# Kernel tuning notes

Hardware: AMD Instinct MI355X
Metric: run time of the kernel (lower is better)

The kernel has to match this reference:

```python
import jax, jax.numpy as jnp
import numpy as np
import math

L, B, S, D, H, DI, V = 4, 2, 1024, 768, 12, 3072, 512
DK = D // H

def gelu_tanh(x):
    c = math.sqrt(2.0 / math.pi)
    return 0.5 * x * (1.0 + jnp.tanh(c * (x + 0.044715 * x ** 3)))

def layer_norm(x, g, b, eps=1e-5):
    mu = jnp.mean(x, axis=-1, keepdims=True)
    var = jnp.var(x, axis=-1, keepdims=True)
    return (x - mu) * jax.lax.rsqrt(var + eps) * g + b

def setup_inputs() -> dict:
    key = jax.random.key(0)
    ks = jax.random.split(key, 12)
    w = 0.02  # init scale
    return {
        "x": jax.random.randint(ks[0], (B, S), 0, V),
        "embed": jax.random.normal(ks[1], (V, D), jnp.float32) * w,
        "pos_emb": jax.random.normal(ks[2], (S, D), jnp.float32) * w,
        "ln1_g": jnp.ones((L, D), jnp.float32),
        "ln1_b": jnp.zeros((L, D), jnp.float32),
        "wq": jax.random.normal(ks[3], (L, D, D), jnp.float32) * w,
        "bq": jnp.zeros((L, D), jnp.float32),
        "wk": jax.random.normal(ks[4], (L, D, D), jnp.float32) * w,
        "bk": jnp.zeros((L, D), jnp.float32),
        "wv": jax.random.normal(ks[5], (L, D, D), jnp.float32) * w,
        "bv": jnp.zeros((L, D), jnp.float32),
        "wo": jax.random.normal(ks[6], (L, D, D), jnp.float32) * w,
        "bo": jnp.zeros((L, D), jnp.float32),
        "ln2_g": jnp.ones((L, D), jnp.float32),
        "ln2_b": jnp.zeros((L, D), jnp.float32),
        "w_in": jax.random.normal(ks[7], (L, D, DI), jnp.float32) * w,
        "b_in": jnp.zeros((L, DI), jnp.float32),
        "w_out": jax.random.normal(ks[8], (L, DI, D), jnp.float32) * w,
        "b_out": jnp.zeros((L, D), jnp.float32),
        "lnf_g": jnp.ones((D,), jnp.float32),
        "lnf_b": jnp.zeros((D,), jnp.float32),
        "out_w": jax.random.normal(ks[9], (D, V), jnp.float32) * w,
    }

def reference(x, embed, pos_emb, ln1_g, ln1_b, wq, bq, wk, bk, wv, bv, wo, bo,
              ln2_g, ln2_b, w_in, b_in, w_out, b_out, lnf_g, lnf_b, out_w):
    s = x.shape[1]
    h = embed[x] + pos_emb[None, :s]                       # [B,S,D]
    causal = jnp.tril(jnp.ones((s, s), bool))              # True = keep
    scale = 1.0 / math.sqrt(DK)
    for l in range(L):
        a = layer_norm(h, ln1_g[l], ln1_b[l])
        q = (a @ wq[l] + bq[l]).reshape(-1, s, H, DK)
        k = (a @ wk[l] + bk[l]).reshape(-1, s, H, DK)
        v = (a @ wv[l] + bv[l]).reshape(-1, s, H, DK)
        scores = jnp.einsum('bqhd,bkhd->bhqk', q, k) * scale
        scores = jnp.where(causal, scores, -jnp.inf)
        attn = jax.nn.softmax(scores, axis=-1)
        o = jnp.einsum('bhqk,bkhd->bqhd', attn, v).reshape(-1, s, D)
        h = h + o @ wo[l] + bo[l]
        f = layer_norm(h, ln2_g[l], ln2_b[l])
        h = h + gelu_tanh(f @ w_in[l] + b_in[l]) @ w_out[l] + b_out[l]
    h = layer_norm(h, lnf_g, lnf_b)
    return h @ out_w                                       # [B,S,V] logits
```

## Files before the change

kernel.cpp:

```cpp
#include <hip/hip_runtime.h>
#include <hip/hip_bf16.h>


#define TKN    2048
#define DMODEL 768
#define SEQ    1024
#define NH     12
#define DHEAD  64
#define DFF    3072
#define NL     4
#define NVOCAB 512
#define NQKV   2304

typedef unsigned short u16;
typedef __attribute__((ext_vector_type(4))) float f32x4;
typedef __attribute__((ext_vector_type(8))) short short8;
typedef __attribute__((ext_vector_type(4))) unsigned short us4;

__device__ __forceinline__ u16 f2bf(float f) {
  unsigned u = __builtin_bit_cast(unsigned, f);
  u += 0x7fffu + ((u >> 16) & 1u);
  return (u16)(u >> 16);
}

__device__ __forceinline__ float bf2f(u16 u) {
  unsigned v = ((unsigned)u) << 16;
  return __builtin_bit_cast(float, v);
}

__device__ __forceinline__ u16 bf_eighth(u16 u) {
  int e = (u >> 7) & 0xFF;
  return e >= 3 ? (u16)(u - (3 << 7)) : (u16)(u & 0x8000);
}

__device__ __forceinline__ short8 mk8(us4 lo, us4 hi) {
  short8 r;
  r[0] = (short)lo[0]; r[1] = (short)lo[1]; r[2] = (short)lo[2]; r[3] = (short)lo[3];
  r[4] = (short)hi[0]; r[5] = (short)hi[1]; r[6] = (short)hi[2]; r[7] = (short)hi[3];
  return r;
}

__device__ __forceinline__ void gload16(const u16* g, u16* l) {
  __builtin_amdgcn_global_load_lds(
      (const __attribute__((address_space(1))) unsigned int*)g,
      (__attribute__((address_space(3))) unsigned int*)l, 16, 0, 0);
}

__global__ __launch_bounds__(256) void k_embed(const int* __restrict__ x,
                                               const float* __restrict__ emb,
                                               const float* __restrict__ pos,
                                               float* __restrict__ h) {
  int t = blockIdx.x;
  int s = t & (SEQ - 1);
  int id = x[t];
  int d = threadIdx.x;
#pragma unroll
  for (int j = 0; j < 3; ++j, d += 256)
    h[t * DMODEL + d] = emb[id * DMODEL + d] + pos[s * DMODEL + d];
}

__global__ __launch_bounds__(256) void k_ln(const float* __restrict__ h,
                                            const float* __restrict__ gam,
                                            const float* __restrict__ bet,
                                            u16* __restrict__ out) {
  __shared__ float sbuf[8];
  int row = blockIdx.x, tid = threadIdx.x;
  const float* hr = h + (size_t)row * DMODEL;
  float x0 = hr[tid], x1 = hr[tid + 256], x2 = hr[tid + 512];
  float s = x0 + x1 + x2;
#pragma unroll
  for (int off = 32; off > 0; off >>= 1) s += __shfl_down(s, off);
  if ((tid & 63) == 0) sbuf[tid >> 6] = s;
  __syncthreads();
  float mu = (sbuf[0] + sbuf[1] + sbuf[2] + sbuf[3]) * (1.0f / DMODEL);
  float d0 = x0 - mu, d1 = x1 - mu, d2 = x2 - mu;
  float v = d0 * d0 + d1 * d1 + d2 * d2;
#pragma unroll
  for (int off = 32; off > 0; off >>= 1) v += __shfl_down(v, off);
  if ((tid & 63) == 0) sbuf[4 + (tid >> 6)] = v;
  __syncthreads();
  float var = (sbuf[4] + sbuf[5] + sbuf[6] + sbuf[7]) * (1.0f / DMODEL);
  float rstd = rsqrtf(var + 1e-5f);
  size_t o = (size_t)row * DMODEL;
  out[o + tid]       = f2bf(d0 * rstd * gam[tid]       + bet[tid]);
  out[o + tid + 256] = f2bf(d1 * rstd * gam[tid + 256] + bet[tid + 256]);
  out[o + tid + 512] = f2bf(d2 * rstd * gam[tid + 512] + bet[tid + 512]);
}

__device__ __forceinline__ void cvt_tile(const float* __restrict__ src, int ldS,
                                         int k0, int n0src,
                                         u16* __restrict__ dst, int ldD, int n0dst,
                                         int tid, u16 (*tl)[72]) {
  int kr = tid >> 2, nj = (tid & 3) << 4;
  const float* sp = src + (size_t)(k0 + kr) * ldS + n0src + nj;
  float4 a0 = ((const float4*)sp)[0];
  float4 a1 = ((const float4*)sp)[1];
  float4 a2 = ((const float4*)sp)[2];
  float4 a3 = ((const float4*)sp)[3];
  u16* tr = &tl[kr][nj];
  tr[0]=f2bf(a0.x); tr[1]=f2bf(a0.y); tr[2]=f2bf(a0.z); tr[3]=f2bf(a0.w);
  tr[4]=f2bf(a1.x); tr[5]=f2bf(a1.y); tr[6]=f2bf(a1.z); tr[7]=f2bf(a1.w);
  tr[8]=f2bf(a2.x); tr[9]=f2bf(a2.y); tr[10]=f2bf(a2.z); tr[11]=f2bf(a2.w);
  tr[12]=f2bf(a3.x); tr[13]=f2bf(a3.y); tr[14]=f2bf(a3.z); tr[15]=f2bf(a3.w);
  __syncthreads();
  int nr = tid >> 2, kj = (tid & 3) << 4;
  us4 o[4];
#pragma unroll
  for (int c = 0; c < 4; ++c)
#pragma unroll
    for (int i = 0; i < 4; ++i) o[c][i] = tl[kj + c * 4 + i][nr];
  u16* dp = dst + (size_t)(n0dst + nr) * ldD + k0 + kj;
  ((us4*)dp)[0] = o[0]; ((us4*)dp)[1] = o[1];
  ((us4*)dp)[2] = o[2]; ((us4*)dp)[3] = o[3];
}

__global__ __launch_bounds__(256) void k_cvtL(const float* __restrict__ wq,
                                              const float* __restrict__ wk,
                                              const float* __restrict__ wv,
                                              const float* __restrict__ wo,
                                              const float* __restrict__ win,
                                              const float* __restrict__ wout,
                                              u16* __restrict__ wqkvT,
                                              u16* __restrict__ woT,
                                              u16* __restrict__ winT,
                                              u16* __restrict__ woutT) {
  __shared__ u16 tl[64][72];
  int t = blockIdx.x, tid = threadIdx.x;
  if (t < 432) {
    int kt = t % 12, ntile = t / 12;
    int gn0 = ntile * 64, sel = gn0 / DMODEL;
    const float* src = sel == 0 ? wq : sel == 1 ? wk : wv;
    cvt_tile(src, DMODEL, kt * 64, gn0 - sel * DMODEL, wqkvT, DMODEL, gn0, tid, tl);
  } else if (t < 576) {
    int t2 = t - 432, kt = t2 % 12, nt = t2 / 12;
    cvt_tile(wo, DMODEL, kt * 64, nt * 64, woT, DMODEL, nt * 64, tid, tl);
  } else if (t < 1152) {
    int t3 = t - 576, kt = t3 % 12, nt = t3 / 12;
    cvt_tile(win, DFF, kt * 64, nt * 64, winT, DMODEL, nt * 64, tid, tl);
  } else {
    int t4 = t - 1152, kt = t4 % 48, nt = t4 / 48;
    cvt_tile(wout, DMODEL, kt * 64, nt * 64, woutT, DFF, nt * 64, tid, tl);
  }
}

__global__ __launch_bounds__(256) void k_cvtT(const float* __restrict__ src,
                                              u16* __restrict__ dst,
                                              int K, int N) {
  __shared__ u16 tl[64][72];
  cvt_tile(src, N, blockIdx.x * 64, blockIdx.y * 64, dst, K, blockIdx.y * 64,
           threadIdx.x, tl);
}

__global__ __launch_bounds__(256) void k_packb(const float* __restrict__ bq,
                                               const float* __restrict__ bk,
                                               const float* __restrict__ bv,
                                               float* __restrict__ dst) {
  int i = blockIdx.x * 256 + threadIdx.x;
  if (i < NL * NQKV) {
    int l = i / NQKV, j = i - l * NQKV;
    float v = j < DMODEL ? bq[l * DMODEL + j]
            : j < 2 * DMODEL ? bk[l * DMODEL + j - DMODEL]
            : bv[l * DMODEL + j - 2 * DMODEL];
    dst[i] = v;
  }
}

template <int EP, int BM, int BN>
__global__ __launch_bounds__(256) void k_mm(const u16* __restrict__ A,
                                            const u16* __restrict__ BT,
                                            const float* __restrict__ bias,
                                            void* __restrict__ outp,
                                            int N, int K) {
  constexpr int MI = BM / 32;
  constexpr int NJ = BN / 32;
  __shared__ __align__(16) u16 As[2][BM * 64];
  __shared__ __align__(16) u16 Bs[2][BN * 64];
  const int nbx = gridDim.x;
  int lin = blockIdx.y * nbx + blockIdx.x;
  const int chunk = (nbx * gridDim.y) >> 3;
  lin = (lin & 7) * chunk + (lin >> 3);
  const int bn = (lin % nbx) * BN, bm = (lin / nbx) * BM;

  const int tid = threadIdx.x, lane = tid & 63, wid = tid >> 6;
  const int g = lane >> 4, fl = lane & 15;
  const int wm = wid >> 1, wn = wid & 1;

  const int srow = wid * 8 + (lane >> 3);
  const int scol = ((lane & 7) ^ (lane >> 3)) << 3;
  const u16* ag = A + (size_t)(bm + srow) * K + scol;
  const u16* bg = BT + (size_t)(bn + srow) * K + scol;

  f32x4 acc[MI][NJ] = {};
  const int sw = (fl & 7) << 4;

  auto stage = [&](int buf, int kk) {
#pragma unroll
    for (int is = 0; is < MI; ++is)
      gload16(ag + kk + (size_t)is * 32 * K, &As[buf][wid * 512 + is * 2048]);
#pragma unroll
    for (int is = 0; is < NJ; ++is)
      gload16(bg + kk + (size_t)is * 32 * K, &Bs[buf][wid * 512 + is * 2048]);
  };

  const int ks = K / gridDim.z;
  const int kb0 = blockIdx.z * ks;
  const int nk = ks >> 6;
  stage(0, kb0);
  __syncthreads();
  int cur = 0;
  for (int kt = 0; kt < nk; ++kt) {
    if (kt + 1 < nk) stage(cur ^ 1, kb0 + ((kt + 1) << 6));
#pragma unroll
    for (int k0 = 0; k0 < 64; k0 += 32) {
      const int bo = (k0 + 4 * g) * 2;
      short8 af[MI], bf[NJ];
#pragma unroll
      for (int i = 0; i < MI; ++i) {
        const char* base = (const char*)&As[cur][(wm * (BM / 2) + i * 16 + fl) * 64];
        af[i] = mk8(*(const us4*)(base + (bo ^ sw)),
                    *(const us4*)(base + ((bo + 32) ^ sw)));
      }
#pragma unroll
      for (int j = 0; j < NJ; ++j) {
        const char* base = (const char*)&Bs[cur][(wn * (BN / 2) + j * 16 + fl) * 64];
        bf[j] = mk8(*(const us4*)(base + (bo ^ sw)),
                    *(const us4*)(base + ((bo + 32) ^ sw)));
      }
#pragma unroll
      for (int i = 0; i < MI; ++i)
#pragma unroll
        for (int j = 0; j < NJ; ++j)
          acc[i][j] = __builtin_amdgcn_mfma_f32_16x16x32_bf16(af[i], bf[j], acc[i][j], 0, 0, 0);
    }
    __syncthreads();
    cur ^= 1;
  }

  const int row0 = bm + wm * (BM / 2) + 4 * g;
  const int col0 = bn + wn * (BN / 2) + fl;
#pragma unroll
  for (int j = 0; j < NJ; ++j) {
    int col = col0 + j * 16;
    float bv = (EP == 3) ? 0.0f : bias[col];
    if (EP == 1 && blockIdx.z != 0) bv = 0.0f;
#pragma unroll
    for (int i = 0; i < MI; ++i) {
#pragma unroll
      for (int r = 0; r < 4; ++r) {
        int row = row0 + i * 16 + r;
        float val = acc[i][j][r] + bv;
        size_t idx = (size_t)row * N + col;
        if (EP == 0) {
          ((u16*)outp)[idx] = f2bf(val);
        } else if (EP == 1) {
          atomicAdd(&((float*)outp)[idx], val);
        } else if (EP == 2) {
          float t = 0.7978845608028654f * (val + 0.044715f * val * val * val);
          ((u16*)outp)[idx] = f2bf(0.5f * val * (1.0f + tanhf(t)));
        } else {
          ((float*)outp)[idx] = val;
        }
      }
    }
  }
}

__global__ __launch_bounds__(256) void k_attn(const u16* __restrict__ qkv,
                                              u16* __restrict__ pO,
                                              float* __restrict__ pML) {
  __shared__ u16 Vt[2][DHEAD * 68];
  int bid = blockIdx.x;
  int lin = (bid & 7) * 120 + (bid >> 3);
  const int bh = lin / 40;
  const int idx = lin - bh * 40;
  int qb, sp;
  if (idx < 4)       { qb = idx;                     sp = 0; }
  else if (idx < 12) { qb = 4 + ((idx - 4) >> 1);    sp = (idx - 4) & 1; }
  else if (idx < 24) { int t = idx - 12; qb = 8 + t / 3;  sp = t - (t / 3) * 3; }
  else               { int t = idx - 24; qb = 12 + (t >> 2); sp = t & 3; }
  const int nsp = 1 + (qb >> 2), nt = qb + 1;
  const int t_lo = sp * nt / nsp, t_hi = (sp + 1) * nt / nsp;

  const int b = bh / NH, hh = bh % NH;
  const int tid = threadIdx.x, lane = tid & 63, w = tid >> 6;
  const int g = lane >> 4, fl = lane & 15;
  const int qrow = qb * 64 + w * 16 + fl;
  const u16* qp = qkv + (size_t)(b * SEQ + qrow) * NQKV + hh * DHEAD;

  short8 qf[2];
#pragma unroll
  for (int hf = 0; hf < 2; ++hf) {
    us4 lo = *(const us4*)(qp + hf * 32 + 4 * g);
    us4 hi = *(const us4*)(qp + hf * 32 + 16 + 4 * g);
#pragma unroll
    for (int i = 0; i < 4; ++i) { lo[i] = bf_eighth(lo[i]); hi[i] = bf_eighth(hi[i]); }
    qf[hf] = mk8(lo, hi);
  }

  float m = -1e30f, lsum = 0.0f;
  f32x4 oacc[4] = {};
  const int vr = tid >> 2, vd = (tid & 3) << 4;
  const u16* vbase = qkv + (size_t)(b * SEQ + vr) * NQKV + 2 * DMODEL + hh * DHEAD + vd;
  const u16* kbase0 = qkv + (size_t)(b * SEQ) * NQKV + DMODEL + hh * DHEAD;

  {
    const u16* vp = vbase + (size_t)t_lo * 64 * NQKV;
    us4 vv[4];
#pragma unroll
    for (int qi = 0; qi < 4; ++qi) vv[qi] = *(const us4*)(vp + qi * 4);
#pragma unroll
    for (int qi = 0; qi < 4; ++qi)
#pragma unroll
      for (int i = 0; i < 4; ++i) Vt[0][(vd + qi * 4 + i) * 68 + vr] = vv[qi][i];
  }
  __syncthreads();
  int cur = 0;

  for (int t64 = t_lo; t64 < t_hi; ++t64) {
    const u16* kb64 = kbase0 + (size_t)t64 * 64 * NQKV;
    us4 kv[4][4];
#pragma unroll
    for (int q4 = 0; q4 < 4; ++q4) {
      const u16* kp = kb64 + (size_t)(q4 * 16 + fl) * NQKV;
#pragma unroll
      for (int j = 0; j < 4; ++j) kv[q4][j] = *(const us4*)(kp + j * 16 + 4 * g);
    }
    const bool pf = (t64 + 1 < t_hi);
    us4 vvn[4];
    if (pf) {
      const u16* vp = vbase + (size_t)(t64 + 1) * 64 * NQKV;
#pragma unroll
      for (int qi = 0; qi < 4; ++qi) vvn[qi] = *(const us4*)(vp + qi * 4);
    }

    f32x4 sfr[4];
    __builtin_amdgcn_s_setprio(1);
#pragma unroll
    for (int sub = 0; sub < 4; ++sub) {
      short8 kf0 = mk8(kv[sub][0], kv[sub][1]);
      short8 kf1 = mk8(kv[sub][2], kv[sub][3]);
      f32x4 s = {};
      s = __builtin_amdgcn_mfma_f32_16x16x32_bf16(kf0, qf[0], s, 0, 0, 0);
      s = __builtin_amdgcn_mfma_f32_16x16x32_bf16(kf1, qf[1], s, 0, 0, 0);
      sfr[sub] = s;
    }
    __builtin_amdgcn_s_setprio(0);

    float sc[16];
    if (t64 == qb) {
#pragma unroll
      for (int sub = 0; sub < 4; ++sub)
#pragma unroll
        for (int r = 0; r < 4; ++r) {
          int key = t64 * 64 + sub * 16 + 4 * g + r;
          sc[sub * 4 + r] = (key <= qrow) ? sfr[sub][r] : -1e30f;
        }
    } else {
#pragma unroll
      for (int sub = 0; sub < 4; ++sub)
#pragma unroll
        for (int r = 0; r < 4; ++r) sc[sub * 4 + r] = sfr[sub][r];
    }
    float pmax = sc[0];
#pragma unroll
    for (int e = 1; e < 16; ++e) pmax = fmaxf(pmax, sc[e]);
    pmax = fmaxf(pmax, __shfl_xor(pmax, 16));
    pmax = fmaxf(pmax, __shfl_xor(pmax, 32));

    float p[16];
    if (__all(pmax <= m + 8.0f)) {
      float ps = 0.0f;
#pragma unroll
      for (int e = 0; e < 16; ++e) { p[e] = __expf(sc[e] - m); ps += p[e]; }
      ps += __shfl_xor(ps, 16);
      ps += __shfl_xor(ps, 32);
      lsum += ps;
    } else {
      float mnew = fmaxf(m, pmax);
      float corr = __expf(m - mnew);
      float ps = 0.0f;
#pragma unroll
      for (int e = 0; e < 16; ++e) { p[e] = __expf(sc[e] - mnew); ps += p[e]; }
      ps += __shfl_xor(ps, 16);
      ps += __shfl_xor(ps, 32);
      lsum = lsum * corr + ps;
      m = mnew;
      float cr[4];
#pragma unroll
      for (int r = 0; r < 4; ++r) cr[r] = __shfl(corr, 4 * g + r);
#pragma unroll
      for (int nb = 0; nb < 4; ++nb)
#pragma unroll
        for (int r = 0; r < 4; ++r) oacc[nb][r] *= cr[r];
    }

    short8 pf0, pf1;
#pragma unroll
    for (int e = 0; e < 8; ++e) { pf0[e] = (short)f2bf(p[e]); pf1[e] = (short)f2bf(p[8 + e]); }

    __builtin_amdgcn_s_setprio(1);
#pragma unroll
    for (int nb = 0; nb < 4; ++nb) {
      const u16* vtp = &Vt[cur][(nb * 16 + fl) * 68 + 4 * g];
      short8 vf0 = mk8(*(const us4*)vtp, *(const us4*)(vtp + 16));
      short8 vf1 = mk8(*(const us4*)(vtp + 32), *(const us4*)(vtp + 48));
      oacc[nb] = __builtin_amdgcn_mfma_f32_16x16x32_bf16(pf0, vf0, oacc[nb], 0, 0, 0);
      oacc[nb] = __builtin_amdgcn_mfma_f32_16x16x32_bf16(pf1, vf1, oacc[nb], 0, 0, 0);
    }
    __builtin_amdgcn_s_setprio(0);

    if (pf) {
      __syncthreads();
#pragma unroll
      for (int qi = 0; qi < 4; ++qi)
#pragma unroll
        for (int i = 0; i < 4; ++i) Vt[cur ^ 1][(vd + qi * 4 + i) * 68 + vr] = vvn[qi][i];
      __syncthreads();
      cur ^= 1;
    }
  }

  const size_t part = ((size_t)bh * 16 + qb) * 4 + sp;
  u16* ob = pO + part * 4096;
  float* ml = pML + part * 128;
#pragma unroll
  for (int nb = 0; nb < 4; ++nb)
#pragma unroll
    for (int r = 0; r < 4; ++r)
      ob[(w * 16 + 4 * g + r) * 64 + nb * 16 + fl] = f2bf(oacc[nb][r]);
  if (g == 0) {
    ml[w * 16 + fl] = m;
    ml[64 + w * 16 + fl] = lsum;
  }
}

__global__ __launch_bounds__(256) void k_ared(const u16* __restrict__ pO,
                                              const float* __restrict__ pML,
                                              u16* __restrict__ O) {
  __shared__ float wgt[4][64];
  __shared__ float iLs[64];
  const int qb = blockIdx.x, bh = blockIdx.y;
  const int nsp = 1 + (qb >> 2);
  const int b = bh / NH, hh = bh % NH;
  const int tid = threadIdx.x;
  const size_t p0 = ((size_t)bh * 16 + qb) * 4;
  if (tid < 64) {
    float M = -1e30f;
    for (int s = 0; s < nsp; ++s) M = fmaxf(M, pML[(p0 + s) * 128 + tid]);
    float L = 0.0f;
    for (int s = 0; s < nsp; ++s) {
      float wv = __expf(pML[(p0 + s) * 128 + tid] - M);
      wgt[s][tid] = wv;
      L += pML[(p0 + s) * 128 + 64 + tid] * wv;
    }
    iLs[tid] = 1.0f / L;
  }
  __syncthreads();
  for (int i = tid; i < 4096; i += 256) {
    int row = i >> 6, d = i & 63;
    float acc = 0.0f;
    for (int s = 0; s < nsp; ++s)
      acc += bf2f(pO[(p0 + s) * 4096 + i]) * wgt[s][row];
    O[(size_t)(b * SEQ + qb * 64 + row) * DMODEL + hh * DHEAD + d] = f2bf(acc * iLs[row]);
  }
}

extern "C" void kernel_launch(void* const* d_in, const int* in_sizes, int n_in,
                              void* d_out, int out_size, void* d_ws, size_t ws_size,
                              hipStream_t stream) {
  const int*   x    = (const int*)d_in[0];
  const float* emb  = (const float*)d_in[1];
  const float* pos  = (const float*)d_in[2];
  const float* ln1g = (const float*)d_in[3];
  const float* ln1b = (const float*)d_in[4];
  const float* wq   = (const float*)d_in[5];
  const float* bq   = (const float*)d_in[6];
  const float* wk   = (const float*)d_in[7];
  const float* bk   = (const float*)d_in[8];
  const float* wv   = (const float*)d_in[9];
  const float* bv   = (const float*)d_in[10];
  const float* wo   = (const float*)d_in[11];
  const float* bo   = (const float*)d_in[12];
  const float* ln2g = (const float*)d_in[13];
  const float* ln2b = (const float*)d_in[14];
  const float* win  = (const float*)d_in[15];
  const float* bin  = (const float*)d_in[16];
  const float* wout = (const float*)d_in[17];
  const float* bout = (const float*)d_in[18];
  const float* lnfg = (const float*)d_in[19];
  const float* lnfb = (const float*)d_in[20];
  const float* outw = (const float*)d_in[21];

  char* w8 = (char*)d_ws;
  float* h    = (float*)(w8);
  u16* abuf   = (u16*)(w8 + 6291456);
  u16* qkv    = (u16*)(w8 + 9437184);
  u16* obuf   = (u16*)(w8 + 18874368);
  u16* ffbuf  = (u16*)(w8 + 9437184);
  u16* wqkvT  = (u16*)(w8 + 22020096);
  u16* woT    = (u16*)(w8 + 25559040);
  u16* winT   = (u16*)(w8 + 26738688);
  u16* woutT  = (u16*)(w8 + 31457280);
  u16* outwT  = (u16*)(w8 + 36175872);
  float* bqkv = (float*)(w8 + 36962304);
  u16* pO     = (u16*)(w8 + 36999168);
  float* pML  = (float*)(w8 + 6291456 + 0);

  pML = (float*)(w8 + 6291456);

  k_embed<<<TKN, 256, 0, stream>>>(x, emb, pos, h);
  k_packb<<<36, 256, 0, stream>>>(bq, bk, bv, bqkv);
  k_cvtT<<<dim3(12, 8), 256, 0, stream>>>(outw, outwT, DMODEL, NVOCAB);

  for (int l = 0; l < NL; ++l) {
    k_cvtL<<<1728, 256, 0, stream>>>(
        wq + (size_t)l * DMODEL * DMODEL, wk + (size_t)l * DMODEL * DMODEL,
        wv + (size_t)l * DMODEL * DMODEL, wo + (size_t)l * DMODEL * DMODEL,
        win + (size_t)l * DMODEL * DFF, wout + (size_t)l * DFF * DMODEL,
        wqkvT, woT, winT, woutT);

    k_ln<<<TKN, 256, 0, stream>>>(h, ln1g + l * DMODEL, ln1b + l * DMODEL, abuf);
    k_mm<0, 128, 64><<<dim3(NQKV / 64, TKN / 128, 1), 256, 0, stream>>>(
        abuf, wqkvT, bqkv + l * NQKV, qkv, NQKV, DMODEL);
    k_attn<<<960, 256, 0, stream>>>(qkv, pO, pML);
    k_ared<<<dim3(SEQ / 64, 2 * NH), 256, 0, stream>>>(pO, pML, obuf);
    k_mm<1, 128, 64><<<dim3(DMODEL / 64, TKN / 128, 2), 256, 0, stream>>>(
        obuf, woT, bo + l * DMODEL, h, DMODEL, DMODEL);
    k_ln<<<TKN, 256, 0, stream>>>(h, ln2g + l * DMODEL, ln2b + l * DMODEL, abuf);
    k_mm<2, 128, 64><<<dim3(DFF / 64, TKN / 128, 1), 256, 0, stream>>>(
        abuf, winT, bin + l * DFF, ffbuf, DFF, DMODEL);
    k_mm<1, 128, 64><<<dim3(DMODEL / 64, TKN / 128, 4), 256, 0, stream>>>(
        ffbuf, woutT, bout + l * DMODEL, h, DMODEL, DFF);
  }

  k_ln<<<TKN, 256, 0, stream>>>(h, lnfg, lnfb, abuf);
  k_mm<3, 64, 64><<<dim3(NVOCAB / 64, TKN / 64, 1), 256, 0, stream>>>(
      abuf, outwT, nullptr, d_out, NVOCAB, DMODEL);
}
```

Measured before the change: 713.3 us.

## Head-major QKV layout, finer attention split, batched weight conversion, single V buffer

The QKV GEMM epilogue now writes Q, K and V into separate head-major [b,h,s,64] buffers and folds the 1/8 softmax scale into Q, so attention no longer rescales Q per element and reads contiguous rows. Attention splits the KV range more finely (up to 8 partials per query block, 1728 blocks) to balance causal work, and the V tile drops from double-buffered to a single LDS buffer. Weight conversion for all layers is hoisted into one launch before the loop, which removes three launches but needs a larger workspace. The single V buffer may add stalls, and the extra partials add reduction traffic.

```diff
diff --git a/kernel.cpp b/kernel.cpp
--- a/kernel.cpp
+++ b/kernel.cpp
@@ -26,11 +26,6 @@
 __device__ __forceinline__ float bf2f(u16 u) {
   unsigned v = ((unsigned)u) << 16;
   return __builtin_bit_cast(float, v);
-}
-
-__device__ __forceinline__ u16 bf_eighth(u16 u) {
-  int e = (u >> 7) & 0xFF;
-  return e >= 3 ? (u16)(u - (3 << 7)) : (u16)(u & 0x8000);
 }
 
 __device__ __forceinline__ short8 mk8(us4 lo, us4 hi) {
@@ -125,21 +120,27 @@
                                               u16* __restrict__ winT,
                                               u16* __restrict__ woutT) {
   __shared__ u16 tl[64][72];
+  const int l = blockIdx.y;
+  const size_t wDD = (size_t)DMODEL * DMODEL, wDF = (size_t)DMODEL * DFF;
   int t = blockIdx.x, tid = threadIdx.x;
   if (t < 432) {
     int kt = t % 12, ntile = t / 12;
     int gn0 = ntile * 64, sel = gn0 / DMODEL;
-    const float* src = sel == 0 ? wq : sel == 1 ? wk : wv;
-    cvt_tile(src, DMODEL, kt * 64, gn0 - sel * DMODEL, wqkvT, DMODEL, gn0, tid, tl);
+    const float* src = (sel == 0 ? wq : sel == 1 ? wk : wv) + l * wDD;
+    cvt_tile(src, DMODEL, kt * 64, gn0 - sel * DMODEL,
+             wqkvT + l * (size_t)NQKV * DMODEL, DMODEL, gn0, tid, tl);
   } else if (t < 576) {
     int t2 = t - 432, kt = t2 % 12, nt = t2 / 12;
-    cvt_tile(wo, DMODEL, kt * 64, nt * 64, woT, DMODEL, nt * 64, tid, tl);
+    cvt_tile(wo + l * wDD, DMODEL, kt * 64, nt * 64,
+             woT + l * wDD, DMODEL, nt * 64, tid, tl);
   } else if (t < 1152) {
     int t3 = t - 576, kt = t3 % 12, nt = t3 / 12;
-    cvt_tile(win, DFF, kt * 64, nt * 64, winT, DMODEL, nt * 64, tid, tl);
+    cvt_tile(win + l * wDF, DFF, kt * 64, nt * 64,
+             winT + l * wDF, DMODEL, nt * 64, tid, tl);
   } else {
     int t4 = t - 1152, kt = t4 % 48, nt = t4 / 48;
-    cvt_tile(wout, DMODEL, kt * 64, nt * 64, woutT, DFF, nt * 64, tid, tl);
+    cvt_tile(wout + l * wDF, DMODEL, kt * 64, nt * 64,
+             woutT + l * wDF, DFF, nt * 64, tid, tl);
   }
 }
 
@@ -257,78 +258,91 @@
         } else if (EP == 2) {
           float t = 0.7978845608028654f * (val + 0.044715f * val * val * val);
           ((u16*)outp)[idx] = f2bf(0.5f * val * (1.0f + tanhf(t)));
+        } else if (EP == 3) {
+          ((float*)outp)[idx] = val;
         } else {
-          ((float*)outp)[idx] = val;
+          int sel = col / DMODEL;
+          int c = col - sel * DMODEL;
+          int hh2 = c >> 6, dk = c & 63;
+          int bb = row >> 10, ss = row & (SEQ - 1);
+          if (sel == 0) val *= 0.125f;
+          ((u16*)outp)[(size_t)sel * (TKN * DMODEL) +
+                       (((size_t)(bb * NH + hh2) * SEQ + ss) << 6) + dk] = f2bf(val);
         }
       }
     }
   }
 }
 
-__global__ __launch_bounds__(256) void k_attn(const u16* __restrict__ qkv,
+__global__ __launch_bounds__(256) void k_attn(const u16* __restrict__ qh,
                                               u16* __restrict__ pO,
                                               float* __restrict__ pML) {
-  __shared__ u16 Vt[2][DHEAD * 68];
+  __shared__ u16 Vt[DHEAD * 68];
   int bid = blockIdx.x;
-  int lin = (bid & 7) * 120 + (bid >> 3);
-  const int bh = lin / 40;
-  const int idx = lin - bh * 40;
-  int qb, sp;
-  if (idx < 4)       { qb = idx;                     sp = 0; }
-  else if (idx < 12) { qb = 4 + ((idx - 4) >> 1);    sp = (idx - 4) & 1; }
-  else if (idx < 24) { int t = idx - 12; qb = 8 + t / 3;  sp = t - (t / 3) * 3; }
-  else               { int t = idx - 24; qb = 12 + (t >> 2); sp = t & 3; }
-  const int nsp = 1 + (qb >> 2), nt = qb + 1;
+  int lin = (bid & 7) * 216 + (bid >> 3);
+  const int bh = lin / 72;
+  const int idx = lin - bh * 72;
+  int qb = 0, sp = 0, c = 0;
+#pragma unroll
+  for (int q = 0; q < 16; ++q) {
+    int n = 1 + (q >> 1);
+    if (idx >= c && idx < c + n) { qb = q; sp = idx - c; }
+    c += n;
+  }
+  const int nsp = 1 + (qb >> 1), nt = qb + 1;
   const int t_lo = sp * nt / nsp, t_hi = (sp + 1) * nt / nsp;
 
   const int b = bh / NH, hh = bh % NH;
+  const u16* kh = qh + TKN * DMODEL;
+  const u16* vh = qh + 2 * (TKN * DMODEL);
+  const size_t headbase = ((size_t)bh * SEQ) << 6;
+
   const int tid = threadIdx.x, lane = tid & 63, w = tid >> 6;
   const int g = lane >> 4, fl = lane & 15;
   const int qrow = qb * 64 + w * 16 + fl;
-  const u16* qp = qkv + (size_t)(b * SEQ + qrow) * NQKV + hh * DHEAD;
 
   short8 qf[2];
-#pragma unroll
-  for (int hf = 0; hf < 2; ++hf) {
-    us4 lo = *(const us4*)(qp + hf * 32 + 4 * g);
-    us4 hi = *(const us4*)(qp + hf * 32 + 16 + 4 * g);
-#pragma unroll
-    for (int i = 0; i < 4; ++i) { lo[i] = bf_eighth(lo[i]); hi[i] = bf_eighth(hi[i]); }
-    qf[hf] = mk8(lo, hi);
+  {
+    const u16* qp = qh + headbase + ((size_t)qrow << 6);
+#pragma unroll
+    for (int hf = 0; hf < 2; ++hf) {
+      us4 lo = *(const us4*)(qp + hf * 32 + 4 * g);
+      us4 hi = *(const us4*)(qp + hf * 32 + 16 + 4 * g);
+      qf[hf] = mk8(lo, hi);
+    }
   }
 
   float m = -1e30f, lsum = 0.0f;
   f32x4 oacc[4] = {};
   const int vr = tid >> 2, vd = (tid & 3) << 4;
-  const u16* vbase = qkv + (size_t)(b * SEQ + vr) * NQKV + 2 * DMODEL + hh * DHEAD + vd;
-  const u16* kbase0 = qkv + (size_t)(b * SEQ) * NQKV + DMODEL + hh * DHEAD;
+  const u16* vbase = vh + headbase + ((size_t)vr << 6) + vd;
+  const u16* kbase = kh + headbase;
 
   {
-    const u16* vp = vbase + (size_t)t_lo * 64 * NQKV;
+    const u16* vp = vbase + ((size_t)t_lo << 12);
     us4 vv[4];
 #pragma unroll
     for (int qi = 0; qi < 4; ++qi) vv[qi] = *(const us4*)(vp + qi * 4);
 #pragma unroll
     for (int qi = 0; qi < 4; ++qi)
 #pragma unroll
-      for (int i = 0; i < 4; ++i) Vt[0][(vd + qi * 4 + i) * 68 + vr] = vv[qi][i];
+      for (int i = 0; i < 4; ++i) Vt[(vd + qi * 4 + i) * 68 + vr] = vv[qi][i];
   }
   __syncthreads();
-  int cur = 0;
 
   for (int t64 = t_lo; t64 < t_hi; ++t64) {
-    const u16* kb64 = kbase0 + (size_t)t64 * 64 * NQKV;
+    const u16* kb64 = kbase + ((size_t)t64 << 12);
     us4 kv[4][4];
 #pragma unroll
     for (int q4 = 0; q4 < 4; ++q4) {
-      const u16* kp = kb64 + (size_t)(q4 * 16 + fl) * NQKV;
+      const u16* kp = kb64 + ((q4 * 16 + fl) << 6);
 #pragma unroll
       for (int j = 0; j < 4; ++j) kv[q4][j] = *(const us4*)(kp + j * 16 + 4 * g);
     }
     const bool pf = (t64 + 1 < t_hi);
     us4 vvn[4];
     if (pf) {
-      const u16* vp = vbase + (size_t)(t64 + 1) * 64 * NQKV;
+      const u16* vp = vbase + ((size_t)(t64 + 1) << 12);
 #pragma unroll
       for (int qi = 0; qi < 4; ++qi) vvn[qi] = *(const us4*)(vp + qi * 4);
     }
@@ -401,7 +415,7 @@
     __builtin_amdgcn_s_setprio(1);
 #pragma unroll
     for (int nb = 0; nb < 4; ++nb) {
-      const u16* vtp = &Vt[cur][(nb * 16 + fl) * 68 + 4 * g];
+      const u16* vtp = &Vt[(nb * 16 + fl) * 68 + 4 * g];
       short8 vf0 = mk8(*(const us4*)vtp, *(const us4*)(vtp + 16));
       short8 vf1 = mk8(*(const us4*)(vtp + 32), *(const us4*)(vtp + 48));
       oacc[nb] = __builtin_amdgcn_mfma_f32_16x16x32_bf16(pf0, vf0, oacc[nb], 0, 0, 0);
@@ -414,13 +428,12 @@
 #pragma unroll
       for (int qi = 0; qi < 4; ++qi)
 #pragma unroll
-        for (int i = 0; i < 4; ++i) Vt[cur ^ 1][(vd + qi * 4 + i) * 68 + vr] = vvn[qi][i];
+        for (int i = 0; i < 4; ++i) Vt[(vd + qi * 4 + i) * 68 + vr] = vvn[qi][i];
       __syncthreads();
-      cur ^= 1;
-    }
-  }
-
-  const size_t part = ((size_t)bh * 16 + qb) * 4 + sp;
+    }
+  }
+
+  const size_t part = ((size_t)bh * 16 + qb) * 8 + sp;
   u16* ob = pO + part * 4096;
   float* ml = pML + part * 128;
 #pragma unroll
@@ -437,13 +450,13 @@
 __global__ __launch_bounds__(256) void k_ared(const u16* __restrict__ pO,
                                               const float* __restrict__ pML,
                                               u16* __restrict__ O) {
-  __shared__ float wgt[4][64];
+  __shared__ float wgt[8][64];
   __shared__ float iLs[64];
   const int qb = blockIdx.x, bh = blockIdx.y;
-  const int nsp = 1 + (qb >> 2);
+  const int nsp = 1 + (qb >> 1);
   const int b = bh / NH, hh = bh % NH;
   const int tid = threadIdx.x;
-  const size_t p0 = ((size_t)bh * 16 + qb) * 4;
+  const size_t p0 = ((size_t)bh * 16 + qb) * 8;
   if (tid < 64) {
     float M = -1e30f;
     for (int s = 0; s < nsp; ++s) M = fmaxf(M, pML[(p0 + s) * 128 + tid]);
@@ -494,43 +507,40 @@
   char* w8 = (char*)d_ws;
   float* h    = (float*)(w8);
   u16* abuf   = (u16*)(w8 + 6291456);
-  u16* qkv    = (u16*)(w8 + 9437184);
+  float* pML  = (float*)(w8 + 6291456);
+  u16* qkvh   = (u16*)(w8 + 9437184);
+  u16* ffbuf  = (u16*)(w8 + 9437184);
   u16* obuf   = (u16*)(w8 + 18874368);
-  u16* ffbuf  = (u16*)(w8 + 9437184);
-  u16* wqkvT  = (u16*)(w8 + 22020096);
-  u16* woT    = (u16*)(w8 + 25559040);
-  u16* winT   = (u16*)(w8 + 26738688);
-  u16* woutT  = (u16*)(w8 + 31457280);
-  u16* outwT  = (u16*)(w8 + 36175872);
-  float* bqkv = (float*)(w8 + 36962304);
-  u16* pO     = (u16*)(w8 + 36999168);
-  float* pML  = (float*)(w8 + 6291456 + 0);
-
-  pML = (float*)(w8 + 6291456);
+  u16* outwT  = (u16*)(w8 + 22020096);
+  float* bqkv = (float*)(w8 + 22806528);
+  u16* pO     = (u16*)(w8 + 22843392);
+  u16* wqkvT  = (u16*)(w8 + 48009216);
+  u16* woT    = (u16*)(w8 + 62164992);
+  u16* winT   = (u16*)(w8 + 66883584);
+  u16* woutT  = (u16*)(w8 + 85757952);
+
+  const size_t wDD = (size_t)DMODEL * DMODEL, wDF = (size_t)DMODEL * DFF;
+  const size_t wQKV = (size_t)NQKV * DMODEL;
 
   k_embed<<<TKN, 256, 0, stream>>>(x, emb, pos, h);
   k_packb<<<36, 256, 0, stream>>>(bq, bk, bv, bqkv);
   k_cvtT<<<dim3(12, 8), 256, 0, stream>>>(outw, outwT, DMODEL, NVOCAB);
+  k_cvtL<<<dim3(1728, NL), 256, 0, stream>>>(wq, wk, wv, wo, win, wout,
+                                             wqkvT, woT, winT, woutT);
 
   for (int l = 0; l < NL; ++l) {
-    k_cvtL<<<1728, 256, 0, stream>>>(
-        wq + (size_t)l * DMODEL * DMODEL, wk + (size_t)l * DMODEL * DMODEL,
-        wv + (size_t)l * DMODEL * DMODEL, wo + (size_t)l * DMODEL * DMODEL,
-        win + (size_t)l * DMODEL * DFF, wout + (size_t)l * DFF * DMODEL,
-        wqkvT, woT, winT, woutT);
-
     k_ln<<<TKN, 256, 0, stream>>>(h, ln1g + l * DMODEL, ln1b + l * DMODEL, abuf);
-    k_mm<0, 128, 64><<<dim3(NQKV / 64, TKN / 128, 1), 256, 0, stream>>>(
-        abuf, wqkvT, bqkv + l * NQKV, qkv, NQKV, DMODEL);
-    k_attn<<<960, 256, 0, stream>>>(qkv, pO, pML);
+    k_mm<4, 128, 64><<<dim3(NQKV / 64, TKN / 128, 1), 256, 0, stream>>>(
+        abuf, wqkvT + l * wQKV, bqkv + l * NQKV, qkvh, NQKV, DMODEL);
+    k_attn<<<1728, 256, 0, stream>>>(qkvh, pO, pML);
     k_ared<<<dim3(SEQ / 64, 2 * NH), 256, 0, stream>>>(pO, pML, obuf);
     k_mm<1, 128, 64><<<dim3(DMODEL / 64, TKN / 128, 2), 256, 0, stream>>>(
-        obuf, woT, bo + l * DMODEL, h, DMODEL, DMODEL);
+        obuf, woT + l * wDD, bo + l * DMODEL, h, DMODEL, DMODEL);
     k_ln<<<TKN, 256, 0, stream>>>(h, ln2g + l * DMODEL, ln2b + l * DMODEL, abuf);
     k_mm<2, 128, 64><<<dim3(DFF / 64, TKN / 128, 1), 256, 0, stream>>>(
-        abuf, winT, bin + l * DFF, ffbuf, DFF, DMODEL);
+        abuf, winT + l * wDF, bin + l * DFF, ffbuf, DFF, DMODEL);
     k_mm<1, 128, 64><<<dim3(DMODEL / 64, TKN / 128, 4), 256, 0, stream>>>(
-        ffbuf, woutT, bout + l * DMODEL, h, DMODEL, DFF);
+        ffbuf, woutT + l * wDF, bout + l * DMODEL, h, DMODEL, DFF);
   }
 
   k_ln<<<TKN, 256, 0, stream>>>(h, lnfg, lnfb, abuf);
```

After: 761.8 us. 1.07x slower.
